# Kernel optimization log

Hardware: AMD Instinct MI355X
Metric: run time of the kernel (lower is better)

## Reference

```python
import jax, jax.numpy as jnp
import numpy as np

CH = 64
INTER = 8  # max(64 // 8, 1)


def setup_inputs() -> dict:
    key = jax.random.key(0)
    ks = jax.random.split(key, 8)
    B, C, H, W = 4, CH, 64, 64
    x = jax.random.normal(ks[0], (B, C, H, W), dtype=jnp.float32)
    s = 1.0 / np.sqrt(C)
    Wq = jax.random.normal(ks[1], (INTER, C), dtype=jnp.float32) * s
    bq = jnp.zeros((INTER,), dtype=jnp.float32)
    Wk = jax.random.normal(ks[2], (INTER, C), dtype=jnp.float32) * s
    bk = jnp.zeros((INTER,), dtype=jnp.float32)
    Wv = jax.random.normal(ks[3], (C, C), dtype=jnp.float32) * s
    bv = jnp.zeros((C,), dtype=jnp.float32)
    gamma = jax.random.normal(ks[4], (1,), dtype=jnp.float32) * 0.1
    return {"x": x, "Wq": Wq, "bq": bq, "Wk": Wk, "bk": bk, "Wv": Wv, "bv": bv, "gamma": gamma}


def reference(x, Wq, bq, Wk, bk, Wv, bv, gamma):
    B, C, H, W = x.shape
    xf = x.reshape(B, C, H * W)  # [B, C, N]
    # 1x1 convs == per-pixel linear projections
    q = jnp.einsum('dc,bcn->bdn', Wq, xf) + bq[None, :, None]  # [B, d, N]
    k = jnp.einsum('dc,bcn->bdn', Wk, xf) + bk[None, :, None]  # [B, d, N]
    v = jnp.einsum('ec,bcn->ben', Wv, xf) + bv[None, :, None]  # [B, C, N]
    scale = 1.0 / np.sqrt(INTER).astype(np.float32)
    scores = jnp.einsum('bdi,bdj->bij', q, k) * scale  # [B, N, N]
    attn = jax.nn.softmax(scores, axis=-1)
    out = jnp.einsum('bcj,bij->bci', v, attn)  # value @ attn^T
    out = out.reshape(B, C, H, W)
    return gamma[0] * out + x
```

## Files before the change

kernel.cpp:

```cpp
#include <hip/hip_runtime.h>
#include <hip/hip_bf16.h>
#include <stdint.h>

#define BATCH 4
#define CCH   64
#define NPIX  4096
#define DQK   8

typedef __attribute__((ext_vector_type(8)))  short bf16x8;
typedef __attribute__((ext_vector_type(16))) float f32x16;
typedef __attribute__((ext_vector_type(4)))  uint32_t u32x4;

static __device__ __forceinline__ short f2bf(float f) {
    union { __hip_bfloat16 h; short s; } u;
    u.h = __float2bfloat16(f);
    return u.s;
}
static __device__ __forceinline__ uint32_t cvt_pk_bf16(float lo, float hi) {
    uint32_t r;
    asm("v_cvt_pk_bf16_f32 %0, %1, %2" : "=v"(r) : "v"(lo), "v"(hi));
    return r;
}

__global__ __launch_bounds__(256) void proj_kernel(
    const float* __restrict__ x,
    const float* __restrict__ Wq, const float* __restrict__ bq,
    const float* __restrict__ Wk, const float* __restrict__ bk,
    const float* __restrict__ Wv, const float* __restrict__ bv,
    short* __restrict__ qo, short* __restrict__ ko, short* __restrict__ vo)
{
    __shared__ float xs[CCH][32];
    __shared__ float wv_s[CCH][68];
    __shared__ float wq_s[CCH][DQK];
    __shared__ float wk_s[CCH][DQK];

    const int b  = blockIdx.x >> 7;
    const int n0 = (blockIdx.x & 127) << 5;
    const int tid = threadIdx.x;

    for (int i = tid; i < CCH*CCH; i += 256) wv_s[i & 63][i >> 6] = Wv[i];
    for (int i = tid; i < CCH*DQK; i += 256) { wq_s[i & 63][i >> 6] = Wq[i]; wk_s[i & 63][i >> 6] = Wk[i]; }
    for (int i = tid; i < CCH*32; i += 256) {
        int c = i >> 5, p = i & 31;
        xs[c][p] = x[((size_t)b*CCH + c)*NPIX + n0 + p];
    }
    __syncthreads();

    const int p = tid & 31;
    const int g = tid >> 5;
    const int e0 = g * 8;

    float av[8];
    #pragma unroll
    for (int i = 0; i < 8; ++i) av[i] = bv[e0 + i];
    float aq = bq[g], akk = bk[g];

    for (int c = 0; c < CCH; ++c) {
        float xv = xs[c][p];
        float4 w0 = *(const float4*)&wv_s[c][e0];
        float4 w1 = *(const float4*)&wv_s[c][e0 + 4];
        av[0] += w0.x*xv; av[1] += w0.y*xv; av[2] += w0.z*xv; av[3] += w0.w*xv;
        av[4] += w1.x*xv; av[5] += w1.y*xv; av[6] += w1.z*xv; av[7] += w1.w*xv;
        aq  += wq_s[c][g]*xv;
        akk += wk_s[c][g]*xv;
    }

    const float qscale = 0.51010407112635f;
    const size_t vb = (size_t)b * CCH * NPIX;
    #pragma unroll
    for (int i = 0; i < 8; ++i)
        vo[vb + (size_t)(e0 + i)*NPIX + n0 + p] = f2bf(av[i]);
    const size_t qb = ((size_t)b*NPIX + n0 + p)*16 + g;
    qo[qb]     = f2bf(aq * qscale);
    qo[qb + 8] = 0;
    ko[qb]     = f2bf(akk);
    ko[qb + 8] = 0;
}

__global__ __launch_bounds__(512, 2) void attn_kernel(
    const short* __restrict__ qg, const short* __restrict__ kg,
    const short* __restrict__ vg,
    const float* __restrict__ x, const float* __restrict__ gamma,
    float* __restrict__ outp)
{
    __shared__ float l_s[8][32];
    __shared__ float linv_s[32];
    __shared__ float acc_all[8][CCH][32];

    const int b  = blockIdx.x >> 7;
    const int i0 = (blockIdx.x & 127) << 5;
    const int tid  = threadIdx.x;
    const int wave = tid >> 6, lane = tid & 63;
    const int hi = lane >> 5, li = lane & 31;

    f32x16 z16;
    #pragma unroll
    for (int r = 0; r < 16; ++r) z16[r] = 0.f;

    const bf16x8 qf = *(const bf16x8*)&qg[((size_t)b*NPIX + i0 + li)*16 + hi*8];

    f32x16 acc0 = z16, acc1 = z16;
    float l_run = 0.f;

    const short* kp = kg + (size_t)b * NPIX * 16;
    const size_t vbase = (size_t)b * CCH * NPIX;
    const short* vrow0 = &vg[vbase + (size_t)li*NPIX];
    const short* vrow1 = vrow0 + (size_t)32*NPIX;

    const int jbeg = wave << 9;
    #pragma unroll 2
    for (int t = 0; t < 16; ++t) {
        const int j0 = jbeg + t*32;

        bf16x8 akf = *(const bf16x8*)&kp[(size_t)(j0 + li)*16 + hi*8];
        f32x16 S = __builtin_amdgcn_mfma_f32_32x32x16_bf16(akf, qf, z16, 0, 0, 0);

        bf16x8 av00 = *(const bf16x8*)(vrow0 + j0 + hi*8);
        bf16x8 av01 = *(const bf16x8*)(vrow0 + j0 + 16 + hi*8);
        bf16x8 av10 = *(const bf16x8*)(vrow1 + j0 + hi*8);
        bf16x8 av11 = *(const bf16x8*)(vrow1 + j0 + 16 + hi*8);

        #pragma unroll
        for (int r = 0; r < 16; ++r) S[r] = __builtin_amdgcn_exp2f(S[r]);

        {
            float s0 = (S[0]+S[1]) + (S[2]+S[3]);
            float s1 = (S[4]+S[5]) + (S[6]+S[7]);
            float s2 = (S[8]+S[9]) + (S[10]+S[11]);
            float s3 = (S[12]+S[13]) + (S[14]+S[15]);
            l_run += (s0+s1) + (s2+s3);
        }

        uint32_t a01 = cvt_pk_bf16(S[0], S[1]);
        uint32_t a23 = cvt_pk_bf16(S[2], S[3]);
        uint32_t a45 = cvt_pk_bf16(S[4], S[5]);
        uint32_t a67 = cvt_pk_bf16(S[6], S[7]);
        uint32_t a89 = cvt_pk_bf16(S[8], S[9]);
        uint32_t aab = cvt_pk_bf16(S[10], S[11]);
        uint32_t acd = cvt_pk_bf16(S[12], S[13]);
        uint32_t aef = cvt_pk_bf16(S[14], S[15]);
        asm("v_permlane32_swap_b32 %0, %1" : "+v"(a01), "+v"(a45));
        asm("v_permlane32_swap_b32 %0, %1" : "+v"(a23), "+v"(a67));
        asm("v_permlane32_swap_b32 %0, %1" : "+v"(a89), "+v"(acd));
        asm("v_permlane32_swap_b32 %0, %1" : "+v"(aab), "+v"(aef));
        u32x4 pw0 = { a01, a23, a45, a67 };
        u32x4 pw1 = { a89, aab, acd, aef };
        bf16x8 b0 = __builtin_bit_cast(bf16x8, pw0);
        bf16x8 b1 = __builtin_bit_cast(bf16x8, pw1);

        acc0 = __builtin_amdgcn_mfma_f32_32x32x16_bf16(av00, b0, acc0, 0, 0, 0);
        acc1 = __builtin_amdgcn_mfma_f32_32x32x16_bf16(av10, b0, acc1, 0, 0, 0);
        acc0 = __builtin_amdgcn_mfma_f32_32x32x16_bf16(av01, b1, acc0, 0, 0, 0);
        acc1 = __builtin_amdgcn_mfma_f32_32x32x16_bf16(av11, b1, acc1, 0, 0, 0);
    }

    l_run += __shfl_xor(l_run, 32);
    if (hi == 0) l_s[wave][li] = l_run;
    #pragma unroll
    for (int r = 0; r < 16; ++r) {
        int row = (r & 3) + ((r >> 2) << 3) + (hi << 2);
        acc_all[wave][row][li]      = acc0[r];
        acc_all[wave][row + 32][li] = acc1[r];
    }
    __syncthreads();
    if (wave == 0 && hi == 0) {
        float L = 0.f;
        #pragma unroll
        for (int w = 0; w < 8; ++w) L += l_s[w][li];
        linv_s[li] = __builtin_amdgcn_rcpf(L);
    }
    __syncthreads();

    const float g0 = gamma[0];
    for (int idx = tid; idx < CCH*32; idx += 512) {
        int c = idx >> 5, i = idx & 31;
        float s = 0.f;
        #pragma unroll
        for (int w = 0; w < 8; ++w) s += acc_all[w][c][i];
        size_t gidx = vbase + (size_t)c*NPIX + i0 + i;
        outp[gidx] = g0 * (s * linv_s[i]) + x[gidx];
    }
}

extern "C" void kernel_launch(void* const* d_in, const int* in_sizes, int n_in,
                              void* d_out, int out_size, void* d_ws, size_t ws_size,
                              hipStream_t stream) {
    const float* x     = (const float*)d_in[0];
    const float* Wq    = (const float*)d_in[1];
    const float* bq    = (const float*)d_in[2];
    const float* Wk    = (const float*)d_in[3];
    const float* bk    = (const float*)d_in[4];
    const float* Wv    = (const float*)d_in[5];
    const float* bv    = (const float*)d_in[6];
    const float* gamma = (const float*)d_in[7];

    short* qo = (short*)d_ws;
    short* ko = qo + (size_t)BATCH*NPIX*16;
    short* vo = ko + (size_t)BATCH*NPIX*16;

    proj_kernel<<<BATCH*(NPIX/32), 256, 0, stream>>>(x, Wq, bq, Wk, bk, Wv, bv, qo, ko, vo);
    attn_kernel<<<BATCH*(NPIX/32), 512, 0, stream>>>(qo, ko, vo, x, gamma, (float*)d_out);
}
```

Measured before the change: 112.2 us.

## Prefetch next K/V tiles in attention loop and widen projection blocks

The attention loop now software-pipelines its global loads: K and V fragments for the next 32-column tile are issued before the current tile's MFMA, exp and PV work, so load latency overlaps compute. The PV MFMAs are wrapped in s_setprio to favour the matrix issue. The projection kernel processes 128 pixels per block instead of 32, amortising the per-block weight staging into shared memory over four times as many pixels. In exchange, register pressure rises in both kernels, and the last iteration issues a redundant wrapped-around load.

```diff
diff --git a/kernel.cpp b/kernel.cpp
--- a/kernel.cpp
+++ b/kernel.cpp
@@ -6,6 +6,7 @@
 #define CCH   64
 #define NPIX  4096
 #define DQK   8
+#define PXB   128
 
 typedef __attribute__((ext_vector_type(8)))  short bf16x8;
 typedef __attribute__((ext_vector_type(16))) float f32x16;
@@ -29,52 +30,65 @@
     const float* __restrict__ Wv, const float* __restrict__ bv,
     short* __restrict__ qo, short* __restrict__ ko, short* __restrict__ vo)
 {
-    __shared__ float xs[CCH][32];
+    __shared__ float xs[CCH][PXB];
     __shared__ float wv_s[CCH][68];
     __shared__ float wq_s[CCH][DQK];
     __shared__ float wk_s[CCH][DQK];
 
-    const int b  = blockIdx.x >> 7;
-    const int n0 = (blockIdx.x & 127) << 5;
+    const int b  = blockIdx.x >> 5;
+    const int n0 = (blockIdx.x & 31) * PXB;
     const int tid = threadIdx.x;
 
     for (int i = tid; i < CCH*CCH; i += 256) wv_s[i & 63][i >> 6] = Wv[i];
     for (int i = tid; i < CCH*DQK; i += 256) { wq_s[i & 63][i >> 6] = Wq[i]; wk_s[i & 63][i >> 6] = Wk[i]; }
-    for (int i = tid; i < CCH*32; i += 256) {
-        int c = i >> 5, p = i & 31;
+    for (int i = tid; i < CCH*PXB; i += 256) {
+        int c = i >> 7, p = i & 127;
         xs[c][p] = x[((size_t)b*CCH + c)*NPIX + n0 + p];
     }
     __syncthreads();
 
-    const int p = tid & 31;
-    const int g = tid >> 5;
+    const int p0 = tid & 31;
+    const int g  = tid >> 5;
     const int e0 = g * 8;
 
-    float av[8];
-    #pragma unroll
-    for (int i = 0; i < 8; ++i) av[i] = bv[e0 + i];
-    float aq = bq[g], akk = bk[g];
+    float av[4][8];
+    float aq[4], ak[4];
+    #pragma unroll
+    for (int pi = 0; pi < 4; ++pi) {
+        #pragma unroll
+        for (int i = 0; i < 8; ++i) av[pi][i] = bv[e0 + i];
+        aq[pi] = bq[g]; ak[pi] = bk[g];
+    }
 
     for (int c = 0; c < CCH; ++c) {
-        float xv = xs[c][p];
         float4 w0 = *(const float4*)&wv_s[c][e0];
         float4 w1 = *(const float4*)&wv_s[c][e0 + 4];
-        av[0] += w0.x*xv; av[1] += w0.y*xv; av[2] += w0.z*xv; av[3] += w0.w*xv;
-        av[4] += w1.x*xv; av[5] += w1.y*xv; av[6] += w1.z*xv; av[7] += w1.w*xv;
-        aq  += wq_s[c][g]*xv;
-        akk += wk_s[c][g]*xv;
+        float wq = wq_s[c][g], wk = wk_s[c][g];
+        #pragma unroll
+        for (int pi = 0; pi < 4; ++pi) {
+            float xv = xs[c][p0 + 32*pi];
+            av[pi][0] += w0.x*xv; av[pi][1] += w0.y*xv;
+            av[pi][2] += w0.z*xv; av[pi][3] += w0.w*xv;
+            av[pi][4] += w1.x*xv; av[pi][5] += w1.y*xv;
+            av[pi][6] += w1.z*xv; av[pi][7] += w1.w*xv;
+            aq[pi] += wq*xv; ak[pi] += wk*xv;
+        }
     }
 
     const float qscale = 0.51010407112635f;
     const size_t vb = (size_t)b * CCH * NPIX;
     #pragma unroll
-    for (int i = 0; i < 8; ++i)
-        vo[vb + (size_t)(e0 + i)*NPIX + n0 + p] = f2bf(av[i]);
-    const size_t qb = ((size_t)b*NPIX + n0 + p)*16 + g;
-    qo[qb]     = f2bf(aq * qscale);
-    qo[qb + 8] = 0;
-    ko[qb]     = f2bf(akk);
-    ko[qb + 8] = 0;
+    for (int pi = 0; pi < 4; ++pi) {
+        const int px = n0 + p0 + 32*pi;
+        #pragma unroll
+        for (int i = 0; i < 8; ++i)
+            vo[vb + (size_t)(e0 + i)*NPIX + px] = f2bf(av[pi][i]);
+        const size_t qb = ((size_t)b*NPIX + px)*16 + g;
+        qo[qb]     = f2bf(aq[pi] * qscale);
+        qo[qb + 8] = 0;
+        ko[qb]     = f2bf(ak[pi]);
+        ko[qb + 8] = 0;
+    }
 }
 
 __global__ __launch_bounds__(512, 2) void attn_kernel(
@@ -108,17 +122,23 @@
     const short* vrow1 = vrow0 + (size_t)32*NPIX;
 
     const int jbeg = wave << 9;
+
+    bf16x8 kc  = *(const bf16x8*)&kp[(size_t)(jbeg + li)*16 + hi*8];
+    bf16x8 v00 = *(const bf16x8*)(vrow0 + jbeg + hi*8);
+    bf16x8 v01 = *(const bf16x8*)(vrow0 + jbeg + 16 + hi*8);
+    bf16x8 v10 = *(const bf16x8*)(vrow1 + jbeg + hi*8);
+    bf16x8 v11 = *(const bf16x8*)(vrow1 + jbeg + 16 + hi*8);
+
     #pragma unroll 2
     for (int t = 0; t < 16; ++t) {
-        const int j0 = jbeg + t*32;
-
-        bf16x8 akf = *(const bf16x8*)&kp[(size_t)(j0 + li)*16 + hi*8];
-        f32x16 S = __builtin_amdgcn_mfma_f32_32x32x16_bf16(akf, qf, z16, 0, 0, 0);
-
-        bf16x8 av00 = *(const bf16x8*)(vrow0 + j0 + hi*8);
-        bf16x8 av01 = *(const bf16x8*)(vrow0 + j0 + 16 + hi*8);
-        bf16x8 av10 = *(const bf16x8*)(vrow1 + j0 + hi*8);
-        bf16x8 av11 = *(const bf16x8*)(vrow1 + j0 + 16 + hi*8);
+        const int j1 = jbeg + ((t + 1) & 15)*32;
+        bf16x8 kn  = *(const bf16x8*)&kp[(size_t)(j1 + li)*16 + hi*8];
+        bf16x8 n00 = *(const bf16x8*)(vrow0 + j1 + hi*8);
+        bf16x8 n01 = *(const bf16x8*)(vrow0 + j1 + 16 + hi*8);
+        bf16x8 n10 = *(const bf16x8*)(vrow1 + j1 + hi*8);
+        bf16x8 n11 = *(const bf16x8*)(vrow1 + j1 + 16 + hi*8);
+
+        f32x16 S = __builtin_amdgcn_mfma_f32_32x32x16_bf16(kc, qf, z16, 0, 0, 0);
 
         #pragma unroll
         for (int r = 0; r < 16; ++r) S[r] = __builtin_amdgcn_exp2f(S[r]);
@@ -148,10 +168,14 @@
         bf16x8 b0 = __builtin_bit_cast(bf16x8, pw0);
         bf16x8 b1 = __builtin_bit_cast(bf16x8, pw1);
 
-        acc0 = __builtin_amdgcn_mfma_f32_32x32x16_bf16(av00, b0, acc0, 0, 0, 0);
-        acc1 = __builtin_amdgcn_mfma_f32_32x32x16_bf16(av10, b0, acc1, 0, 0, 0);
-        acc0 = __builtin_amdgcn_mfma_f32_32x32x16_bf16(av01, b1, acc0, 0, 0, 0);
-        acc1 = __builtin_amdgcn_mfma_f32_32x32x16_bf16(av11, b1, acc1, 0, 0, 0);
+        __builtin_amdgcn_s_setprio(1);
+        acc0 = __builtin_amdgcn_mfma_f32_32x32x16_bf16(v00, b0, acc0, 0, 0, 0);
+        acc1 = __builtin_amdgcn_mfma_f32_32x32x16_bf16(v10, b0, acc1, 0, 0, 0);
+        acc0 = __builtin_amdgcn_mfma_f32_32x32x16_bf16(v01, b1, acc0, 0, 0, 0);
+        acc1 = __builtin_amdgcn_mfma_f32_32x32x16_bf16(v11, b1, acc1, 0, 0, 0);
+        __builtin_amdgcn_s_setprio(0);
+
+        kc = kn; v00 = n00; v01 = n01; v10 = n10; v11 = n11;
     }
 
     l_run += __shfl_xor(l_run, 32);
@@ -198,6 +222,6 @@
     short* ko = qo + (size_t)BATCH*NPIX*16;
     short* vo = ko + (size_t)BATCH*NPIX*16;
 
-    proj_kernel<<<BATCH*(NPIX/32), 256, 0, stream>>>(x, Wq, bq, Wk, bk, Wv, bv, qo, ko, vo);
+    proj_kernel<<<BATCH*(NPIX/PXB), 256, 0, stream>>>(x, Wq, bq, Wk, bk, Wv, bv, qo, ko, vo);
     attn_kernel<<<BATCH*(NPIX/32), 512, 0, stream>>>(qo, ko, vo, x, gamma, (float*)d_out);
 }
```

Result: slower. 116.3 us (+3.7%).
